# Kernel tuning notes

Hardware: AMD Instinct MI355X
Metric: run time of the kernel (lower is better)

The kernel has to match this reference:

```python
import jax, jax.numpy as jnp
import numpy as np

B, T, N, D = 16, 16, 256, 384  # batch, timesteps, patches, feature dim
QDIM = 384                      # query_dim
TEMP = 1.0                      # temperature
TOPK = 16                       # topk_k
EPS = 1e-8


def setup_inputs() -> dict:
    key = jax.random.key(0)
    k1, k2, k3, k4, k5, k6 = jax.random.split(key, 6)
    queries = jax.random.normal(k1, (B, T, QDIM), dtype=jnp.float32)
    patch_features = jax.random.normal(k2, (B, T, N, D), dtype=jnp.float32)
    # encoder.query_input_proj: Linear(query_dim -> D)
    W_in = jax.random.normal(k3, (QDIM, D), dtype=jnp.float32) / np.sqrt(QDIM)
    b_in = jax.random.normal(k4, (D,), dtype=jnp.float32) * 0.01
    # encoder.query_output_proj: Linear(D -> dino_dim)
    W_out = jax.random.normal(k5, (D, QDIM), dtype=jnp.float32) / np.sqrt(D)
    b_out = jax.random.normal(k6, (QDIM,), dtype=jnp.float32) * 0.01
    return {"queries": queries, "patch_features": patch_features,
            "W_in": W_in, "b_in": b_in, "W_out": W_out, "b_out": b_out}


def reference(queries, patch_features, W_in, b_in, W_out, b_out):
    # q_proj: [B,T,D]
    q_proj = jnp.einsum('btq,qd->btd', queries, W_in) + b_in
    # scores: [B,T,N]
    scores = jnp.einsum('btd,btnd->btn', q_proj, patch_features) / TEMP
    attn = jax.nn.softmax(scores, axis=-1)
    # top-k hard mask + renormalize
    k = min(TOPK, N)
    vals, idx = jax.lax.top_k(attn, k)                     # [B,T,k]
    bi = jnp.arange(B)[:, None, None]
    ti = jnp.arange(T)[None, :, None]
    attn_hard = jnp.zeros_like(attn).at[bi, ti, idx].set(vals)
    attn = attn_hard / (attn_hard.sum(axis=-1, keepdims=True) + EPS)
    # weighted sum over patches: [B,T,D]
    out = jnp.einsum('btn,btnd->btd', attn, patch_features)
    out = jnp.einsum('btd,dq->btq', out, W_out) + b_out    # [B,T,QDIM]
    return out
```

## Files before the change

### kernel.cpp

```cpp
#include <hip/hip_runtime.h>
#include <math.h>

#define B_  16
#define T_  16
#define N_  256
#define D_  384
#define Q_  384
#define K_  16
#define BT_ (B_ * T_)


__global__ __launch_bounds__(768)
void qproj_kernel(const float* __restrict__ queries,
                  const float* __restrict__ W_in,
                  const float* __restrict__ b_in,
                  float* __restrict__ qp)
{
    const int bt  = blockIdx.x;
    const int tid = threadIdx.x;

    __shared__ __align__(16) float s_q[Q_];
    __shared__ float s_part[2 * D_];

    if (tid < Q_) s_q[tid] = queries[(size_t)bt * Q_ + tid];
    __syncthreads();

    {
        const int half = tid >= D_;
        const int d    = tid - half * D_;
        const int q0   = half * (Q_ / 2);
        float a0 = 0.f, a1 = 0.f, a2 = 0.f, a3 = 0.f;
        #pragma unroll 4
        for (int q = q0; q < q0 + Q_ / 2; q += 4) {
            a0 += s_q[q]     * W_in[(size_t)(q)     * D_ + d];
            a1 += s_q[q + 1] * W_in[(size_t)(q + 1) * D_ + d];
            a2 += s_q[q + 2] * W_in[(size_t)(q + 2) * D_ + d];
            a3 += s_q[q + 3] * W_in[(size_t)(q + 3) * D_ + d];
        }
        s_part[tid] = (a0 + a1) + (a2 + a3);
    }
    __syncthreads();
    if (tid < D_)
        qp[(size_t)bt * D_ + tid] = s_part[tid] + s_part[tid + D_] + b_in[tid];
}

__global__ __launch_bounds__(1024, 4)
void fused_kernel(const float* __restrict__ patch,
                  const float* __restrict__ qp,
                  const float* __restrict__ W_out,
                  const float* __restrict__ b_out,
                  float* __restrict__ out)
{
    const int bt   = blockIdx.x;
    const int tid  = threadIdx.x;
    const int lane = tid & 63;
    const int wave = tid >> 6;

    __shared__ __align__(16) float s_qp[D_];
    __shared__ float s_sc[N_];
    __shared__ int   s_cnt4[N_][4];
    __shared__ float s_red[4];
    __shared__ float s_red2[4][2];
    __shared__ float s_w[K_];
    __shared__ int   s_ix[K_];
    __shared__ float s_part[2 * D_];
    __shared__ float s_od[D_];

    const float* __restrict__ ptile = patch + (size_t)bt * N_ * D_;

    if (tid < D_) s_qp[tid] = qp[(size_t)bt * D_ + tid];
    __syncthreads();

    {
        const int g  = lane >> 4;
        const int sl = lane & 15;
        const int n0 = wave * 4 + g;
        const float4* s_qp4 = reinterpret_cast<const float4*>(s_qp);

        float4 qv[6];
        #pragma unroll
        for (int c = 0; c < 6; ++c) qv[c] = s_qp4[c * 16 + sl];

        float4 A[6], Bu[6];

#define LOADROW(dst, it) {                                                     \
        const float* pr = ptile + (size_t)(n0 + (it) * 64) * D_;               \
        _Pragma("unroll")                                                      \
        for (int c = 0; c < 6; ++c)                                            \
            dst[c] = *reinterpret_cast<const float4*>(pr + c * 64 + 4 * sl); }

#define DOTSTORE(src, it) {                                                    \
        float p = 0.f;                                                         \
        _Pragma("unroll")                                                      \
        for (int c = 0; c < 6; ++c)                                            \
            p += src[c].x * qv[c].x + src[c].y * qv[c].y                       \
               + src[c].z * qv[c].z + src[c].w * qv[c].w;                      \
        _Pragma("unroll")                                                      \
        for (int off = 8; off; off >>= 1) p += __shfl_xor(p, off, 16);         \
        if (sl == 0) s_sc[n0 + (it) * 64] = p; }

        LOADROW(A, 0)
        LOADROW(Bu, 1)
        DOTSTORE(A, 0)
        LOADROW(A, 2)
        DOTSTORE(Bu, 1)
        LOADROW(Bu, 3)
        DOTSTORE(A, 2)
        DOTSTORE(Bu, 3)
#undef LOADROW
#undef DOTSTORE
    }
    __syncthreads();

    if (tid < N_) {
        float v = s_sc[tid];
        #pragma unroll
        for (int off = 32; off; off >>= 1) v = fmaxf(v, __shfl_xor(v, off));
        if (lane == 0) s_red[wave] = v;
    }
    {
        const int i   = tid >> 2;
        const int sub = tid & 3;
        const float si = s_sc[i];
        int c = 0;
        #pragma unroll 8
        for (int j = sub * 64; j < sub * 64 + 64; ++j) {
            const float sj = s_sc[j];
            c += (int)(sj > si) | ((int)(sj == si) & (int)(j < i));
        }
        s_cnt4[i][sub] = c;
    }
    __syncthreads();

    float e = 0.f;
    int   cnt = N_;
    if (tid < N_) {
        const float mx = fmaxf(fmaxf(s_red[0], s_red[1]), fmaxf(s_red[2], s_red[3]));
        cnt = s_cnt4[tid][0] + s_cnt4[tid][1] + s_cnt4[tid][2] + s_cnt4[tid][3];
        e = __expf(s_sc[tid] - mx);

        float z  = e;
        float sk = (cnt < K_) ? e : 0.f;
        #pragma unroll
        for (int off = 32; off; off >>= 1) {
            z  += __shfl_xor(z, off);
            sk += __shfl_xor(sk, off);
        }
        if (lane == 0) { s_red2[wave][0] = z; s_red2[wave][1] = sk; }
    }
    __syncthreads();

    {
        const float Z  = s_red2[0][0] + s_red2[1][0] + s_red2[2][0] + s_red2[3][0];
        const float SK = s_red2[0][1] + s_red2[1][1] + s_red2[2][1] + s_red2[3][1];
        const float inv = 1.f / (SK + 1e-8f * Z);
        if (tid < N_ && cnt < K_) {
            s_ix[cnt] = tid;
            s_w[cnt]  = e * inv;
        }
    }
    __syncthreads();

    if (tid < 2 * D_) {
        const int half = tid >= D_;
        const int d    = tid - half * D_;
        const int j0   = half * (K_ / 2);
        float acc = 0.f;
        #pragma unroll
        for (int j = j0; j < j0 + K_ / 2; ++j)
            acc += s_w[j] * ptile[(size_t)s_ix[j] * D_ + d];
        s_part[tid] = acc;
    }
    __syncthreads();
    if (tid < D_) s_od[tid] = s_part[tid] + s_part[tid + D_];
    __syncthreads();

    if (tid < 2 * Q_) {
        const int half = tid >= Q_;
        const int q    = tid - half * Q_;
        const int d0   = half * (D_ / 2);
        float a0 = 0.f, a1 = 0.f, a2 = 0.f, a3 = 0.f;
        #pragma unroll 4
        for (int d = d0; d < d0 + D_ / 2; d += 4) {
            a0 += s_od[d]     * W_out[(size_t)(d)     * Q_ + q];
            a1 += s_od[d + 1] * W_out[(size_t)(d + 1) * Q_ + q];
            a2 += s_od[d + 2] * W_out[(size_t)(d + 2) * Q_ + q];
            a3 += s_od[d + 3] * W_out[(size_t)(d + 3) * Q_ + q];
        }
        s_part[tid] = (a0 + a1) + (a2 + a3);
    }
    __syncthreads();
    if (tid < Q_)
        out[(size_t)bt * Q_ + tid] = s_part[tid] + s_part[tid + Q_] + b_out[tid];
}

extern "C" void kernel_launch(void* const* d_in, const int* in_sizes, int n_in,
                              void* d_out, int out_size, void* d_ws, size_t ws_size,
                              hipStream_t stream) {
    const float* queries = (const float*)d_in[0];
    const float* patch   = (const float*)d_in[1];
    const float* W_in    = (const float*)d_in[2];
    const float* b_in    = (const float*)d_in[3];
    const float* W_out   = (const float*)d_in[4];
    const float* b_out   = (const float*)d_in[5];
    float* out = (float*)d_out;

    float* qp = (float*)d_ws;

    qproj_kernel<<<dim3(BT_), dim3(768), 0, stream>>>(queries, W_in, b_in, qp);
    fused_kernel<<<dim3(BT_), dim3(1024), 0, stream>>>(patch, qp, W_out, b_out, out);
}
```

Before: 37.86 us.

## Tile qproj over batch rows and deepen patch-load prefetch to three rows

The query projection kernel now gives each block a 128-column by 8-row tile, so every W_in element loaded is reused for two queries per thread and W_in traffic drops. The grid becomes 3x32 blocks instead of 256, and it loads queries with float4. In the fused kernel, three patch rows are now in flight before the first dot product instead of two. This adds more memory-level parallelism at the cost of extra registers under the 1024-thread launch bound.

```diff
diff --git a/kernel.cpp b/kernel.cpp
--- a/kernel.cpp
+++ b/kernel.cpp
@@ -10,38 +10,50 @@
 #define BT_ (B_ * T_)
 
 
-__global__ __launch_bounds__(768)
+#define QP_DT 128
+#define QP_BT 8
+
+__global__ __launch_bounds__(512)
 void qproj_kernel(const float* __restrict__ queries,
                   const float* __restrict__ W_in,
                   const float* __restrict__ b_in,
                   float* __restrict__ qp)
 {
-    const int bt  = blockIdx.x;
+    const int d0  = blockIdx.x * QP_DT;
+    const int bt0 = blockIdx.y * QP_BT;
     const int tid = threadIdx.x;
 
-    __shared__ __align__(16) float s_q[Q_];
-    __shared__ float s_part[2 * D_];
-
-    if (tid < Q_) s_q[tid] = queries[(size_t)bt * Q_ + tid];
-    __syncthreads();
-
-    {
-        const int half = tid >= D_;
-        const int d    = tid - half * D_;
-        const int q0   = half * (Q_ / 2);
-        float a0 = 0.f, a1 = 0.f, a2 = 0.f, a3 = 0.f;
-        #pragma unroll 4
-        for (int q = q0; q < q0 + Q_ / 2; q += 4) {
-            a0 += s_q[q]     * W_in[(size_t)(q)     * D_ + d];
-            a1 += s_q[q + 1] * W_in[(size_t)(q + 1) * D_ + d];
-            a2 += s_q[q + 2] * W_in[(size_t)(q + 2) * D_ + d];
-            a3 += s_q[q + 3] * W_in[(size_t)(q + 3) * D_ + d];
-        }
-        s_part[tid] = (a0 + a1) + (a2 + a3);
-    }
-    __syncthreads();
-    if (tid < D_)
-        qp[(size_t)bt * D_ + tid] = s_part[tid] + s_part[tid + D_] + b_in[tid];
+    __shared__ __align__(16) float s_q[QP_BT][Q_];
+
+    {
+        const float4* src = reinterpret_cast<const float4*>(queries + (size_t)bt0 * Q_);
+        float4* dst = reinterpret_cast<float4*>(&s_q[0][0]);
+        dst[tid] = src[tid];
+        if (tid < 256) dst[tid + 512] = src[tid + 512];
+    }
+    __syncthreads();
+
+    const int dcol = tid & 127;
+    const int r    = tid >> 7;
+    const int d    = d0 + dcol;
+    const int bta  = r * 2;
+    const int btb  = r * 2 + 1;
+
+    float acc0 = 0.f, acc1 = 0.f;
+    #pragma unroll 4
+    for (int q = 0; q < Q_; q += 4) {
+        const float w0 = W_in[(size_t)(q + 0) * D_ + d];
+        const float w1 = W_in[(size_t)(q + 1) * D_ + d];
+        const float w2 = W_in[(size_t)(q + 2) * D_ + d];
+        const float w3 = W_in[(size_t)(q + 3) * D_ + d];
+        const float4 qa = *reinterpret_cast<const float4*>(&s_q[bta][q]);
+        const float4 qb = *reinterpret_cast<const float4*>(&s_q[btb][q]);
+        acc0 += qa.x * w0 + qa.y * w1 + qa.z * w2 + qa.w * w3;
+        acc1 += qb.x * w0 + qb.y * w1 + qb.z * w2 + qb.w * w3;
+    }
+    const float bi = b_in[d];
+    qp[(size_t)(bt0 + bta) * D_ + d] = acc0 + bi;
+    qp[(size_t)(bt0 + btb) * D_ + d] = acc1 + bi;
 }
 
 __global__ __launch_bounds__(1024, 4)
@@ -81,7 +93,7 @@
         #pragma unroll
         for (int c = 0; c < 6; ++c) qv[c] = s_qp4[c * 16 + sl];
 
-        float4 A[6], Bu[6];
+        float4 A[6], Bu[6], C[6];
 
 #define LOADROW(dst, it) {                                                     \
         const float* pr = ptile + (size_t)(n0 + (it) * 64) * D_;               \
@@ -101,12 +113,12 @@
 
         LOADROW(A, 0)
         LOADROW(Bu, 1)
+        LOADROW(C, 2)
         DOTSTORE(A, 0)
-        LOADROW(A, 2)
+        LOADROW(A, 3)
         DOTSTORE(Bu, 1)
-        LOADROW(Bu, 3)
-        DOTSTORE(A, 2)
-        DOTSTORE(Bu, 3)
+        DOTSTORE(C, 2)
+        DOTSTORE(A, 3)
 #undef LOADROW
 #undef DOTSTORE
     }
@@ -207,6 +219,8 @@
 
     float* qp = (float*)d_ws;
 
-    qproj_kernel<<<dim3(BT_), dim3(768), 0, stream>>>(queries, W_in, b_in, qp);
-    fused_kernel<<<dim3(BT_), dim3(1024), 0, stream>>>(patch, qp, W_out, b_out, out);
+    qproj_kernel<<<dim3(D_ / QP_DT, BT_ / QP_BT), dim3(512), 0, stream>>>(
+        queries, W_in, b_in, qp);
+    fused_kernel<<<dim3(BT_), dim3(1024), 0, stream>>>(
+        patch, qp, W_out, b_out, out);
 }
```

Measured after the change: 48.33 us. 1.28x slower.
